# Kernel optimization log

Hardware: AMD Instinct MI355X
Metric: run time of the kernel (lower is better)

## Reference

```python
import math
import jax, jax.numpy as jnp
import numpy as np

T, C, NE = 4096, 2048, 2048
LAYER_ID, NUM_LAYERS = 12, 24


def setup_inputs() -> dict:
    key = jax.random.key(0)
    ks = jax.random.split(key, 5)
    r01 = LAYER_ID / (NUM_LAYERS - 1)
    r1a0 = 1.0 - LAYER_ID / NUM_LAYERS
    idx = jnp.arange(C, dtype=jnp.float32)
    # parameter inits faithful to the haiku module
    time_decay = -5.0 + 8.0 * (idx / (C - 1)) ** (0.7 + 1.3 * r01)
    time_first = jnp.full((C,), math.log(0.3), jnp.float32) + (jnp.mod(idx + 1, 3) - 1.0) * 0.5
    ddd = (idx / C)[None, :]  # [1, C]
    time_mix_k = jnp.power(ddd, r1a0)
    time_mix_v = jnp.power(ddd, r1a0) + 0.3 * r01
    time_mix_r = jnp.power(ddd, r1a0 * 0.5)
    scale = 0.02  # ~ 1/sqrt(fan_in), keeps exp(k) stable
    x = jax.random.normal(ks[0], (T, NE), jnp.float32)
    Wk = jax.random.normal(ks[1], (NE, C), jnp.float32) * scale
    Wv = jax.random.normal(ks[2], (NE, C), jnp.float32) * scale
    Wr = jax.random.normal(ks[3], (NE, C), jnp.float32) * scale
    Wo = jax.random.normal(ks[4], (C, NE), jnp.float32) * scale
    return {"x": x, "time_first": time_first, "time_decay": time_decay,
            "time_mix_k": time_mix_k, "time_mix_v": time_mix_v, "time_mix_r": time_mix_r,
            "Wk": Wk, "Wv": Wv, "Wr": Wr, "Wo": Wo}


def wkv_conv(w, u, k, v):
    # w,u: [C]; k,v: [T,C].  Faithful conv-trick WKV from the source module.
    w = -jnp.exp(w)
    kT, vT = k.T, v.T                      # [C, T]
    ek = jnp.exp(kT)
    a = ek * vT
    Tlen = kT.shape[1]
    Cn = kT.shape[0]
    # depthwise conv kernel: exp(decay * relative position), last tap = exp(u)
    td = jnp.arange(-(Tlen - 2), 1, dtype=kT.dtype)[None, :] * jnp.exp(w)[:, None]  # [C, T-1]
    td = jnp.concatenate([td, u[:, None]], axis=1)                                   # [C, T]
    kernel = jnp.exp(td)[:, None]           # [C, 1, T]
    a3 = jnp.pad(a[None], ((0, 0), (0, 0), (Tlen - 1, 0)))   # [1, C, 2T-1]
    k3 = jnp.pad(ek[None], ((0, 0), (0, 0), (Tlen - 1, 0)))
    num = jax.lax.conv_general_dilated(a3, kernel, (1,), [(0, 0)], feature_group_count=Cn)
    den = jax.lax.conv_general_dilated(k3, kernel, (1,), [(0, 0)], feature_group_count=Cn)
    return (num / den)[0]                   # [C, T]


def reference(x, time_first, time_decay, time_mix_k, time_mix_v, time_mix_r, Wk, Wv, Wr, Wo):
    xx = jnp.pad(x, ((1, 0), (0, 0)))[:-1]          # time shift
    xk = x * time_mix_k + xx * (1.0 - time_mix_k)
    xv = x * time_mix_v + xx * (1.0 - time_mix_v)
    xr = x * time_mix_r + xx * (1.0 - time_mix_r)
    k = xk @ Wk                                     # [T, C]
    v = xv @ Wv
    r = xr @ Wr
    sr = jax.nn.sigmoid(r)
    wkv = wkv_conv(time_decay, time_first, k, v).T  # [T, C]
    return (sr * wkv) @ Wo                          # [T, n_embd]
```

## Files before the change

### kernel.cpp

```cpp
#include <hip/hip_runtime.h>
#include <hip/hip_bf16.h>
#include <cstdint>
#include <cstddef>

#define T_LEN   4096
#define C_DIM   2048
#define NE_DIM  2048
#define CHUNK   64
#define NCHUNK  (T_LEN / CHUNK)

typedef __bf16 bf16;
typedef __attribute__((ext_vector_type(8))) __bf16 bf16x8;
typedef __attribute__((ext_vector_type(4))) __bf16 bf16x4;
typedef __attribute__((ext_vector_type(4))) float  f32x4;

__device__ __forceinline__ void gld_lds16(bf16* lds_dst, const bf16* g_src) {
  __builtin_amdgcn_global_load_lds(
      (__attribute__((address_space(1))) void*)(g_src),
      (__attribute__((address_space(3))) void*)(lds_dst),
      16, 0, 0);
}

__global__ __launch_bounds__(256) void mix_kernel(
    const float* __restrict__ x,
    const float* __restrict__ tmk, const float* __restrict__ tmv,
    const float* __restrict__ tmr,
    bf16* __restrict__ xk, bf16* __restrict__ xv, bf16* __restrict__ xr)
{
  int gid = blockIdx.x * 256 + threadIdx.x;
  int row = gid / (NE_DIM / 4);
  int e4  = gid % (NE_DIM / 4);
  const f32x4* x4 = (const f32x4*)x;
  f32x4 zero = {0.f, 0.f, 0.f, 0.f};
  f32x4 xc = x4[gid];
  f32x4 xp = (row > 0) ? x4[gid - NE_DIM / 4] : zero;
  f32x4 mk = ((const f32x4*)tmk)[e4];
  f32x4 mv = ((const f32x4*)tmv)[e4];
  f32x4 mr = ((const f32x4*)tmr)[e4];
  f32x4 vk = xc * mk + xp * (1.0f - mk);
  f32x4 vv = xc * mv + xp * (1.0f - mv);
  f32x4 vr = xc * mr + xp * (1.0f - mr);
  bf16x4 ok, ov, orr;
#pragma unroll
  for (int i = 0; i < 4; ++i) {
    ok[i]  = (bf16)vk[i];
    ov[i]  = (bf16)vv[i];
    orr[i] = (bf16)vr[i];
  }
  *(bf16x4*)(xk + (size_t)gid * 4) = ok;
  *(bf16x4*)(xv + (size_t)gid * 4) = ov;
  *(bf16x4*)(xr + (size_t)gid * 4) = orr;
}

__global__ __launch_bounds__(256) void wtrans(
    const float* __restrict__ W0, const float* __restrict__ W1,
    const float* __restrict__ W2, const float* __restrict__ W3,
    bf16* __restrict__ O0, bf16* __restrict__ O1,
    bf16* __restrict__ O2, bf16* __restrict__ O3)
{
  __shared__ float tile[32][33];
  int z = blockIdx.z;
  const float* W = (z == 0) ? W0 : (z == 1) ? W1 : (z == 2) ? W2 : W3;
  bf16* O        = (z == 0) ? O0 : (z == 1) ? O1 : (z == 2) ? O2 : O3;
  int bx = blockIdx.x * 32, by = blockIdx.y * 32;
  int tx = threadIdx.x, ty = threadIdx.y;
#pragma unroll
  for (int j = 0; j < 4; ++j)
    tile[ty + j * 8][tx] = W[(size_t)(by + ty + j * 8) * NE_DIM + bx + tx];
  __syncthreads();
#pragma unroll
  for (int j = 0; j < 4; ++j)
    O[(size_t)(bx + ty + j * 8) * NE_DIM + by + tx] = (bf16)tile[tx][ty + j * 8];
}

#define BM 128
#define BN 128
#define BK 32
__global__ __launch_bounds__(256) void gemm_bt(
    const bf16* __restrict__ A, const bf16* __restrict__ Bt,
    float* __restrict__ C, int M, int N, int K)
{
  __shared__ __align__(16) bf16 As[BM * BK];
  __shared__ __align__(16) bf16 Bs[BN * BK];
  int tid = threadIdx.x;
  int bm = blockIdx.y, bn = blockIdx.x;
  int w = tid >> 6, lane = tid & 63;
  int wm = w >> 1, wn = w & 1;
  int lr = lane & 15, kb = lane >> 4;
  f32x4 acc[4][4] = {};

  const bf16* Ab = A  + (size_t)(bm * BM) * K;
  const bf16* Bb = Bt + (size_t)(bn * BN) * K;
  int s0 = tid, s1 = tid + 256;
  int r0 = s0 >> 2, c0 = (s0 & 3) * 8;
  int r1 = s1 >> 2, c1 = (s1 & 3) * 8;

  for (int k0 = 0; k0 < K; k0 += BK) {
    gld_lds16(&As[s0 * 8], Ab + (size_t)r0 * K + k0 + c0);
    gld_lds16(&As[s1 * 8], Ab + (size_t)r1 * K + k0 + c1);
    gld_lds16(&Bs[s0 * 8], Bb + (size_t)r0 * K + k0 + c0);
    gld_lds16(&Bs[s1 * 8], Bb + (size_t)r1 * K + k0 + c1);
    __syncthreads();

    bf16x8 af[4], bfr[4];
#pragma unroll
    for (int mi = 0; mi < 4; ++mi)
      af[mi] = *(const bf16x8*)&As[(wm * 64 + mi * 16 + lr) * BK + kb * 8];
#pragma unroll
    for (int ni = 0; ni < 4; ++ni)
      bfr[ni] = *(const bf16x8*)&Bs[(wn * 64 + ni * 16 + lr) * BK + kb * 8];
#pragma unroll
    for (int mi = 0; mi < 4; ++mi)
#pragma unroll
      for (int ni = 0; ni < 4; ++ni)
        acc[mi][ni] = __builtin_amdgcn_mfma_f32_16x16x32_bf16(
            af[mi], bfr[ni], acc[mi][ni], 0, 0, 0);
    __syncthreads();
  }

#pragma unroll
  for (int mi = 0; mi < 4; ++mi)
#pragma unroll
    for (int ni = 0; ni < 4; ++ni) {
      int rbase = bm * BM + wm * 64 + mi * 16 + kb * 4;
      int col   = bn * BN + wn * 64 + ni * 16 + lr;
#pragma unroll
      for (int j = 0; j < 4; ++j)
        C[(size_t)(rbase + j) * N + col] = acc[mi][ni][j];
    }
}

__global__ __launch_bounds__(256) void wkv_phase1(
    const float* __restrict__ k, const float* __restrict__ v,
    const float* __restrict__ td,
    float* __restrict__ SA, float* __restrict__ SB)
{
  int c = blockIdx.x * 256 + threadIdx.x;
  int m = blockIdx.y;
  float f = __expf(-__expf(td[c]));
  float D = __expf(-f);
  float sa = 0.f, sb = 0.f;
  size_t base = (size_t)m * CHUNK * C_DIM + c;
  for (int t = 0; t < CHUNK; ++t) {
    float ek = __expf(k[base + (size_t)t * C_DIM]);
    float vv = v[base + (size_t)t * C_DIM];
    sa = D * sa + ek * vv;
    sb = D * sb + ek;
  }
  SA[(size_t)m * C_DIM + c] = sa;
  SB[(size_t)m * C_DIM + c] = sb;
}

__global__ __launch_bounds__(256) void wkv_phase2(
    const float* __restrict__ td,
    const float* __restrict__ SA, const float* __restrict__ SB,
    float* __restrict__ A0, float* __restrict__ B0)
{
  int c = blockIdx.x * 256 + threadIdx.x;
  float f  = __expf(-__expf(td[c]));
  float DL = __expf(-f * (float)CHUNK);
  float a = 0.f, b = 0.f;
  for (int m = 0; m < NCHUNK; ++m) {
    A0[(size_t)m * C_DIM + c] = a;
    B0[(size_t)m * C_DIM + c] = b;
    a = DL * a + SA[(size_t)m * C_DIM + c];
    b = DL * b + SB[(size_t)m * C_DIM + c];
  }
}

__global__ __launch_bounds__(256) void wkv_phase3(
    const float* __restrict__ k, const float* __restrict__ v,
    const float* __restrict__ r,
    const float* __restrict__ td, const float* __restrict__ tf,
    const float* __restrict__ A0, const float* __restrict__ B0,
    bf16* __restrict__ y)
{
  int c = blockIdx.x * 256 + threadIdx.x;
  int m = blockIdx.y;
  float f  = __expf(-__expf(td[c]));
  float D  = __expf(-f);
  float eu = __expf(tf[c]);
  float a = A0[(size_t)m * C_DIM + c];
  float b = B0[(size_t)m * C_DIM + c];
  size_t base = (size_t)m * CHUNK * C_DIM + c;
  for (int t = 0; t < CHUNK; ++t) {
    size_t idx = base + (size_t)t * C_DIM;
    float kk = k[idx], vv = v[idx], rr = r[idx];
    float ek  = __expf(kk);
    float euk = eu * ek;
    float wkv = (a + euk * vv) / (b + euk);
    float sr  = 1.0f / (1.0f + __expf(-rr));
    y[idx] = (bf16)(sr * wkv);
    a = D * a + ek * vv;
    b = D * b + ek;
  }
}

extern "C" void kernel_launch(void* const* d_in, const int* in_sizes, int n_in,
                              void* d_out, int out_size, void* d_ws, size_t ws_size,
                              hipStream_t stream)
{
  (void)in_sizes; (void)n_in; (void)out_size; (void)ws_size;
  const float* x   = (const float*)d_in[0];
  const float* tf  = (const float*)d_in[1];
  const float* td  = (const float*)d_in[2];
  const float* tmk = (const float*)d_in[3];
  const float* tmv = (const float*)d_in[4];
  const float* tmr = (const float*)d_in[5];
  const float* Wk  = (const float*)d_in[6];
  const float* Wv  = (const float*)d_in[7];
  const float* Wr  = (const float*)d_in[8];
  const float* Wo  = (const float*)d_in[9];
  float* out = (float*)d_out;

  char* ws = (char*)d_ws;
  size_t off = 0;
  auto alloc = [&](size_t bytes) {
    void* p = ws + off;
    off += (bytes + 255) & ~(size_t)255;
    return p;
  };
  const size_t TN  = (size_t)T_LEN * NE_DIM;
  const size_t WN  = (size_t)C_DIM * NE_DIM;

  bf16* xk  = (bf16*)alloc(TN * 2);
  bf16* xv  = (bf16*)alloc(TN * 2);
  bf16* xr  = (bf16*)alloc(TN * 2);
  bf16* WkT = (bf16*)alloc(WN * 2);
  bf16* WvT = (bf16*)alloc(WN * 2);
  bf16* WrT = (bf16*)alloc(WN * 2);
  bf16* WoT = (bf16*)alloc(WN * 2);
  float* kb = (float*)alloc(TN * 4);
  float* vb = (float*)alloc(TN * 4);
  float* rb = (float*)alloc(TN * 4);
  bf16*  y  = xk;
  float* SA = (float*)xv;
  float* SB = SA + (size_t)NCHUNK * C_DIM;
  float* A0 = SB + (size_t)NCHUNK * C_DIM;
  float* B0 = A0 + (size_t)NCHUNK * C_DIM;

  mix_kernel<<<dim3((unsigned)(TN / 4 / 256)), 256, 0, stream>>>(
      x, tmk, tmv, tmr, xk, xv, xr);
  wtrans<<<dim3(64, 64, 4), dim3(32, 8), 0, stream>>>(
      Wk, Wv, Wr, Wo, WkT, WvT, WrT, WoT);
  dim3 ggrid(NE_DIM / BN, T_LEN / BM);
  gemm_bt<<<ggrid, 256, 0, stream>>>(xk, WkT, kb, T_LEN, C_DIM, NE_DIM);
  gemm_bt<<<ggrid, 256, 0, stream>>>(xv, WvT, vb, T_LEN, C_DIM, NE_DIM);
  gemm_bt<<<ggrid, 256, 0, stream>>>(xr, WrT, rb, T_LEN, C_DIM, NE_DIM);
  wkv_phase1<<<dim3(C_DIM / 256, NCHUNK), 256, 0, stream>>>(kb, vb, td, SA, SB);
  wkv_phase2<<<dim3(C_DIM / 256), 256, 0, stream>>>(td, SA, SB, A0, B0);
  wkv_phase3<<<dim3(C_DIM / 256, NCHUNK), 256, 0, stream>>>(
      kb, vb, rb, td, tf, A0, B0, y);
  gemm_bt<<<ggrid, 256, 0, stream>>>(y, WoT, out, T_LEN, NE_DIM, C_DIM);
}
```

Before: 437.8 us.

## Rewrite GEMM with double-buffered swizzled LDS, batch projections, vectorize WKV scan

Replaces the single-buffered GEMM with a double-buffered BK=64 kernel that uses XOR-swizzled LDS layouts, raw vmcnt/barrier control, setprio around MFMAs, and a blockIdx remap for L2 locality. The three k/v/r projections now run in one batched launch. The WKV phases process two channels per thread with float2 loads, and the chunk length is halved to give more parallel blocks. The new GEMM hardcodes K and N as 2048 and uses more LDS per block, which limits occupancy.

```diff
diff --git a/kernel.cpp b/kernel.cpp
--- a/kernel.cpp
+++ b/kernel.cpp
@@ -6,12 +6,14 @@
 #define T_LEN   4096
 #define C_DIM   2048
 #define NE_DIM  2048
-#define CHUNK   64
+#define CHUNK   32
 #define NCHUNK  (T_LEN / CHUNK)
+#define C2      (C_DIM / 2)
 
 typedef __bf16 bf16;
 typedef __attribute__((ext_vector_type(8))) __bf16 bf16x8;
 typedef __attribute__((ext_vector_type(4))) __bf16 bf16x4;
+typedef __attribute__((ext_vector_type(2))) __bf16 bf16x2;
 typedef __attribute__((ext_vector_type(4))) float  f32x4;
 
 __device__ __forceinline__ void gld_lds16(bf16* lds_dst, const bf16* g_src) {
@@ -73,126 +75,174 @@
     O[(size_t)(bx + ty + j * 8) * NE_DIM + by + tx] = (bf16)tile[tx][ty + j * 8];
 }
 
-#define BM 128
-#define BN 128
-#define BK 32
-__global__ __launch_bounds__(256) void gemm_bt(
-    const bf16* __restrict__ A, const bf16* __restrict__ Bt,
-    float* __restrict__ C, int M, int N, int K)
-{
-  __shared__ __align__(16) bf16 As[BM * BK];
-  __shared__ __align__(16) bf16 Bs[BN * BK];
-  int tid = threadIdx.x;
-  int bm = blockIdx.y, bn = blockIdx.x;
-  int w = tid >> 6, lane = tid & 63;
-  int wm = w >> 1, wn = w & 1;
-  int lr = lane & 15, kb = lane >> 4;
+#define GK  2048
+#define NT2 (GK / 64)
+
+#define BARS() asm volatile("s_barrier" ::: "memory")
+#define VMC(n) asm volatile("s_waitcnt vmcnt(" #n ")" ::: "memory")
+
+#define STG(b, kt) do { \
+  _Pragma("unroll") \
+  for (int q = 0; q < 4; ++q) { \
+    gld_lds16(&As[(b) * 8192 + q * 2048 + tid * 8], Ab + (size_t)(q * 32) * GK + (size_t)(kt) * 64); \
+    gld_lds16(&Bs[(b) * 8192 + q * 2048 + tid * 8], Bb + (size_t)(q * 32) * GK + (size_t)(kt) * 64); \
+  } \
+} while (0)
+
+#define COMPUTE(b) do { \
+  bf16x8 af[4][2], bq[4][2]; \
+  _Pragma("unroll") \
+  for (int f = 0; f < 4; ++f) { \
+    af[f][0] = *(const bf16x8*)&As[(b) * 8192 + aoff[f] + cx0]; \
+    af[f][1] = *(const bf16x8*)&As[(b) * 8192 + aoff[f] + cx1]; \
+    bq[f][0] = *(const bf16x8*)&Bs[(b) * 8192 + boff[f] + cx0]; \
+    bq[f][1] = *(const bf16x8*)&Bs[(b) * 8192 + boff[f] + cx1]; \
+  } \
+  __builtin_amdgcn_s_setprio(1); \
+  _Pragma("unroll") \
+  for (int f = 0; f < 4; ++f) \
+    _Pragma("unroll") \
+    for (int g = 0; g < 4; ++g) { \
+      acc[f][g] = __builtin_amdgcn_mfma_f32_16x16x32_bf16(af[f][0], bq[g][0], acc[f][g], 0, 0, 0); \
+      acc[f][g] = __builtin_amdgcn_mfma_f32_16x16x32_bf16(af[f][1], bq[g][1], acc[f][g], 0, 0, 0); \
+    } \
+  __builtin_amdgcn_s_setprio(0); \
+} while (0)
+
+__global__ __launch_bounds__(256, 2) void gemm2(
+    const bf16* __restrict__ A0p, const bf16* __restrict__ Bt0, float* __restrict__ C0p,
+    const bf16* __restrict__ A1p, const bf16* __restrict__ Bt1, float* __restrict__ C1p,
+    const bf16* __restrict__ A2p, const bf16* __restrict__ Bt2, float* __restrict__ C2p)
+{
+  __shared__ __align__(16) bf16 As[16384];
+  __shared__ __align__(16) bf16 Bs[16384];
+  const int z = blockIdx.y;
+  const bf16* A  = (z == 0) ? A0p : (z == 1) ? A1p : A2p;
+  const bf16* Bt = (z == 0) ? Bt0 : (z == 1) ? Bt1 : Bt2;
+  float*      C  = (z == 0) ? C0p : (z == 1) ? C1p : C2p;
+
+  const int tid  = threadIdx.x;
+  const int lane = tid & 63, w = tid >> 6;
+  const int wm = w >> 1, wn = w & 1;
+  const int lr = lane & 15, kb = lane >> 4;
+
+  int wg = blockIdx.x;
+  int l  = (wg & 7) * 64 + (wg >> 3);
+  int bm = l & 31, bn = l >> 5;
+
+  const int sr = tid >> 3;
+  const int sc = (tid & 7) ^ (sr & 7);
+  const bf16* Ab = A  + ((size_t)(bm * 128) + sr) * GK + sc * 8;
+  const bf16* Bb = Bt + ((size_t)(bn * 128) + sr) * GK + sc * 8;
+
+  const int cx0 = (kb ^ (lr & 7)) * 8;
+  const int cx1 = ((kb ^ (lr & 7)) ^ 4) * 8;
+  int aoff[4], boff[4];
+#pragma unroll
+  for (int f = 0; f < 4; ++f) {
+    aoff[f] = (wm * 64 + f * 16 + lr) * 64;
+    boff[f] = (wn * 64 + f * 16 + lr) * 64;
+  }
+
   f32x4 acc[4][4] = {};
 
-  const bf16* Ab = A  + (size_t)(bm * BM) * K;
-  const bf16* Bb = Bt + (size_t)(bn * BN) * K;
-  int s0 = tid, s1 = tid + 256;
-  int r0 = s0 >> 2, c0 = (s0 & 3) * 8;
-  int r1 = s1 >> 2, c1 = (s1 & 3) * 8;
-
-  for (int k0 = 0; k0 < K; k0 += BK) {
-    gld_lds16(&As[s0 * 8], Ab + (size_t)r0 * K + k0 + c0);
-    gld_lds16(&As[s1 * 8], Ab + (size_t)r1 * K + k0 + c1);
-    gld_lds16(&Bs[s0 * 8], Bb + (size_t)r0 * K + k0 + c0);
-    gld_lds16(&Bs[s1 * 8], Bb + (size_t)r1 * K + k0 + c1);
-    __syncthreads();
-
-    bf16x8 af[4], bfr[4];
-#pragma unroll
-    for (int mi = 0; mi < 4; ++mi)
-      af[mi] = *(const bf16x8*)&As[(wm * 64 + mi * 16 + lr) * BK + kb * 8];
-#pragma unroll
-    for (int ni = 0; ni < 4; ++ni)
-      bfr[ni] = *(const bf16x8*)&Bs[(wn * 64 + ni * 16 + lr) * BK + kb * 8];
-#pragma unroll
-    for (int mi = 0; mi < 4; ++mi)
-#pragma unroll
-      for (int ni = 0; ni < 4; ++ni)
-        acc[mi][ni] = __builtin_amdgcn_mfma_f32_16x16x32_bf16(
-            af[mi], bfr[ni], acc[mi][ni], 0, 0, 0);
-    __syncthreads();
-  }
-
-#pragma unroll
-  for (int mi = 0; mi < 4; ++mi)
-#pragma unroll
-    for (int ni = 0; ni < 4; ++ni) {
-      int rbase = bm * BM + wm * 64 + mi * 16 + kb * 4;
-      int col   = bn * BN + wn * 64 + ni * 16 + lr;
+  STG(0, 0);
+  for (int t = 0; t < NT2 - 1; ++t) {
+    const int cur = t & 1;
+    STG(cur ^ 1, t + 1);
+    VMC(8);
+    BARS();
+    COMPUTE(cur);
+    BARS();
+  }
+  VMC(0);
+  BARS();
+  COMPUTE((NT2 - 1) & 1);
+
+#pragma unroll
+  for (int f = 0; f < 4; ++f)
+#pragma unroll
+    for (int g = 0; g < 4; ++g) {
+      size_t r0 = (size_t)(bm * 128) + wm * 64 + f * 16 + kb * 4;
+      int    c0 = bn * 128 + wn * 64 + g * 16 + lr;
 #pragma unroll
       for (int j = 0; j < 4; ++j)
-        C[(size_t)(rbase + j) * N + col] = acc[mi][ni][j];
+        C[(r0 + j) * C_DIM + c0] = acc[f][g][j];
     }
 }
 
 __global__ __launch_bounds__(256) void wkv_phase1(
-    const float* __restrict__ k, const float* __restrict__ v,
-    const float* __restrict__ td,
-    float* __restrict__ SA, float* __restrict__ SB)
+    const float2* __restrict__ k2, const float2* __restrict__ v2,
+    const float2* __restrict__ td2,
+    float2* __restrict__ SA, float2* __restrict__ SB)
 {
   int c = blockIdx.x * 256 + threadIdx.x;
   int m = blockIdx.y;
-  float f = __expf(-__expf(td[c]));
-  float D = __expf(-f);
-  float sa = 0.f, sb = 0.f;
-  size_t base = (size_t)m * CHUNK * C_DIM + c;
+  float2 td = td2[c];
+  float fx = __expf(-__expf(td.x)), fy = __expf(-__expf(td.y));
+  float Dx = __expf(-fx), Dy = __expf(-fy);
+  float sax = 0.f, say = 0.f, sbx = 0.f, sby = 0.f;
+  size_t base = (size_t)m * CHUNK * C2 + c;
   for (int t = 0; t < CHUNK; ++t) {
-    float ek = __expf(k[base + (size_t)t * C_DIM]);
-    float vv = v[base + (size_t)t * C_DIM];
-    sa = D * sa + ek * vv;
-    sb = D * sb + ek;
-  }
-  SA[(size_t)m * C_DIM + c] = sa;
-  SB[(size_t)m * C_DIM + c] = sb;
+    float2 kk = k2[base + (size_t)t * C2];
+    float2 vv = v2[base + (size_t)t * C2];
+    float ekx = __expf(kk.x), eky = __expf(kk.y);
+    sax = Dx * sax + ekx * vv.x;  sbx = Dx * sbx + ekx;
+    say = Dy * say + eky * vv.y;  sby = Dy * sby + eky;
+  }
+  SA[(size_t)m * C2 + c] = make_float2(sax, say);
+  SB[(size_t)m * C2 + c] = make_float2(sbx, sby);
 }
 
 __global__ __launch_bounds__(256) void wkv_phase2(
-    const float* __restrict__ td,
-    const float* __restrict__ SA, const float* __restrict__ SB,
-    float* __restrict__ A0, float* __restrict__ B0)
+    const float2* __restrict__ td2,
+    const float2* __restrict__ SA, const float2* __restrict__ SB,
+    float2* __restrict__ A0, float2* __restrict__ B0)
 {
   int c = blockIdx.x * 256 + threadIdx.x;
-  float f  = __expf(-__expf(td[c]));
-  float DL = __expf(-f * (float)CHUNK);
-  float a = 0.f, b = 0.f;
+  float2 td = td2[c];
+  float fx = __expf(-__expf(td.x)), fy = __expf(-__expf(td.y));
+  float DLx = __expf(-fx * (float)CHUNK), DLy = __expf(-fy * (float)CHUNK);
+  float ax = 0.f, ay = 0.f, bx = 0.f, by = 0.f;
   for (int m = 0; m < NCHUNK; ++m) {
-    A0[(size_t)m * C_DIM + c] = a;
-    B0[(size_t)m * C_DIM + c] = b;
-    a = DL * a + SA[(size_t)m * C_DIM + c];
-    b = DL * b + SB[(size_t)m * C_DIM + c];
+    A0[(size_t)m * C2 + c] = make_float2(ax, ay);
+    B0[(size_t)m * C2 + c] = make_float2(bx, by);
+    float2 sa = SA[(size_t)m * C2 + c];
+    float2 sb = SB[(size_t)m * C2 + c];
+    ax = DLx * ax + sa.x;  ay = DLy * ay + sa.y;
+    bx = DLx * bx + sb.x;  by = DLy * by + sb.y;
   }
 }
 
 __global__ __launch_bounds__(256) void wkv_phase3(
-    const float* __restrict__ k, const float* __restrict__ v,
-    const float* __restrict__ r,
-    const float* __restrict__ td, const float* __restrict__ tf,
-    const float* __restrict__ A0, const float* __restrict__ B0,
+    const float2* __restrict__ k2, const float2* __restrict__ v2,
+    const float2* __restrict__ r2,
+    const float2* __restrict__ td2, const float2* __restrict__ tf2,
+    const float2* __restrict__ A0, const float2* __restrict__ B0,
     bf16* __restrict__ y)
 {
   int c = blockIdx.x * 256 + threadIdx.x;
   int m = blockIdx.y;
-  float f  = __expf(-__expf(td[c]));
-  float D  = __expf(-f);
-  float eu = __expf(tf[c]);
-  float a = A0[(size_t)m * C_DIM + c];
-  float b = B0[(size_t)m * C_DIM + c];
-  size_t base = (size_t)m * CHUNK * C_DIM + c;
+  float2 td = td2[c], tf = tf2[c];
+  float fx = __expf(-__expf(td.x)), fy = __expf(-__expf(td.y));
+  float Dx = __expf(-fx), Dy = __expf(-fy);
+  float eux = __expf(tf.x), euy = __expf(tf.y);
+  float2 a0 = A0[(size_t)m * C2 + c], b0 = B0[(size_t)m * C2 + c];
+  float ax = a0.x, ay = a0.y, bx = b0.x, by = b0.y;
+  size_t base = (size_t)m * CHUNK * C2 + c;
   for (int t = 0; t < CHUNK; ++t) {
-    size_t idx = base + (size_t)t * C_DIM;
-    float kk = k[idx], vv = v[idx], rr = r[idx];
-    float ek  = __expf(kk);
-    float euk = eu * ek;
-    float wkv = (a + euk * vv) / (b + euk);
-    float sr  = 1.0f / (1.0f + __expf(-rr));
-    y[idx] = (bf16)(sr * wkv);
-    a = D * a + ek * vv;
-    b = D * b + ek;
+    size_t idx = base + (size_t)t * C2;
+    float2 kk = k2[idx], vv = v2[idx], rr = r2[idx];
+    float ekx = __expf(kk.x), eky = __expf(kk.y);
+    float ex = eux * ekx,     ey = euy * eky;
+    float wx = (ax + ex * vv.x) / (bx + ex);
+    float wy = (ay + ey * vv.y) / (by + ey);
+    float sx = 1.0f / (1.0f + __expf(-rr.x));
+    float sy = 1.0f / (1.0f + __expf(-rr.y));
+    bf16x2 o2; o2[0] = (bf16)(sx * wx); o2[1] = (bf16)(sy * wy);
+    *(bf16x2*)&y[idx * 2] = o2;
+    ax = Dx * ax + ekx * vv.x;  bx = Dx * bx + ekx;
+    ay = Dy * ay + eky * vv.y;  by = Dy * by + eky;
   }
 }
 
@@ -223,33 +273,35 @@
   const size_t TN  = (size_t)T_LEN * NE_DIM;
   const size_t WN  = (size_t)C_DIM * NE_DIM;
 
-  bf16* xk  = (bf16*)alloc(TN * 2);
-  bf16* xv  = (bf16*)alloc(TN * 2);
-  bf16* xr  = (bf16*)alloc(TN * 2);
-  bf16* WkT = (bf16*)alloc(WN * 2);
-  bf16* WvT = (bf16*)alloc(WN * 2);
-  bf16* WrT = (bf16*)alloc(WN * 2);
-  bf16* WoT = (bf16*)alloc(WN * 2);
-  float* kb = (float*)alloc(TN * 4);
-  float* vb = (float*)alloc(TN * 4);
-  float* rb = (float*)alloc(TN * 4);
-  bf16*  y  = xk;
-  float* SA = (float*)xv;
-  float* SB = SA + (size_t)NCHUNK * C_DIM;
-  float* A0 = SB + (size_t)NCHUNK * C_DIM;
-  float* B0 = A0 + (size_t)NCHUNK * C_DIM;
+  bf16* xk   = (bf16*)alloc(TN * 2);
+  bf16* xv   = (bf16*)alloc(TN * 2);
+  bf16* xr   = (bf16*)alloc(TN * 2);
+  bf16* WkT  = (bf16*)alloc(WN * 2);
+  bf16* WvT  = (bf16*)alloc(WN * 2);
+  bf16* WrT  = (bf16*)alloc(WN * 2);
+  bf16* WoT  = (bf16*)alloc(WN * 2);
+  float* kbuf = (float*)alloc(TN * 4);
+  float* vbuf = (float*)alloc(TN * 4);
+  float* rbuf = (float*)alloc(TN * 4);
+  bf16*   y  = xk;
+  float2* SA = (float2*)xv;
+  float2* SB = SA + (size_t)NCHUNK * C2;
+  float2* A0 = SB + (size_t)NCHUNK * C2;
+  float2* B0 = A0 + (size_t)NCHUNK * C2;
 
   mix_kernel<<<dim3((unsigned)(TN / 4 / 256)), 256, 0, stream>>>(
       x, tmk, tmv, tmr, xk, xv, xr);
   wtrans<<<dim3(64, 64, 4), dim3(32, 8), 0, stream>>>(
       Wk, Wv, Wr, Wo, WkT, WvT, WrT, WoT);
-  dim3 ggrid(NE_DIM / BN, T_LEN / BM);
-  gemm_bt<<<ggrid, 256, 0, stream>>>(xk, WkT, kb, T_LEN, C_DIM, NE_DIM);
-  gemm_bt<<<ggrid, 256, 0, stream>>>(xv, WvT, vb, T_LEN, C_DIM, NE_DIM);
-  gemm_bt<<<ggrid, 256, 0, stream>>>(xr, WrT, rb, T_LEN, C_DIM, NE_DIM);
-  wkv_phase1<<<dim3(C_DIM / 256, NCHUNK), 256, 0, stream>>>(kb, vb, td, SA, SB);
-  wkv_phase2<<<dim3(C_DIM / 256), 256, 0, stream>>>(td, SA, SB, A0, B0);
-  wkv_phase3<<<dim3(C_DIM / 256, NCHUNK), 256, 0, stream>>>(
-      kb, vb, rb, td, tf, A0, B0, y);
-  gemm_bt<<<ggrid, 256, 0, stream>>>(y, WoT, out, T_LEN, NE_DIM, C_DIM);
-}
+  gemm2<<<dim3(512, 3), 256, 0, stream>>>(
+      xk, WkT, kbuf, xv, WvT, vbuf, xr, WrT, rbuf);
+  wkv_phase1<<<dim3(C2 / 256, NCHUNK), 256, 0, stream>>>(
+      (const float2*)kbuf, (const float2*)vbuf, (const float2*)td, SA, SB);
+  wkv_phase2<<<dim3(C2 / 256), 256, 0, stream>>>(
+      (const float2*)td, SA, SB, A0, B0);
+  wkv_phase3<<<dim3(C2 / 256, NCHUNK), 256, 0, stream>>>(
+      (const float2*)kbuf, (const float2*)vbuf, (const float2*)rbuf,
+      (const float2*)td, (const float2*)tf, A0, B0, y);
+  gemm2<<<dim3(512, 1), 256, 0, stream>>>(
+      y, WoT, out, y, WoT, out, y, WoT, out);
+}
```

Result: faster. 405.0 us (-7.5%).
